# Kernel tuning notes

Hardware: AMD Instinct MI355X
Metric: run time of the kernel (lower is better)

Reference implementation:

```python
import jax, jax.numpy as jnp
import numpy as np
from jax import lax

EPS = 1e-5

def setup_inputs() -> dict:
    key = jax.random.key(0)
    k1, k2, k3 = jax.random.split(key, 3)
    B, S, D, W = 4, 4096, 2048, 4
    x = jax.random.normal(k1, (B, S, D), dtype=jnp.float32)
    norm_weight = jnp.ones((D,), dtype=jnp.float32)
    conv_weight = jax.random.normal(k2, (D, W), dtype=jnp.float32) * (1.0 / np.sqrt(W))
    proj_weight = jax.random.normal(k3, (2, D), dtype=jnp.float32) * (1.0 / np.sqrt(D))
    return {"x": x, "norm_weight": norm_weight, "conv_weight": conv_weight, "proj_weight": proj_weight}

def _rmsnorm(x, w):
    var = jnp.mean(x * x, axis=-1, keepdims=True)
    return x * lax.rsqrt(var + EPS) * w

def _causal_dw_conv_silu(h, conv_weight):
    # h: [B,S,D], conv_weight: [D,W]; causal depthwise conv along seq + silu
    B, S, D = h.shape
    W = conv_weight.shape[-1]
    hc = jnp.transpose(h, (0, 2, 1))                      # [B,D,S]
    hc = jnp.pad(hc, ((0, 0), (0, 0), (W - 1, 0)))        # left-pad for causality
    y = lax.conv_general_dilated(
        hc, conv_weight[:, None, :], window_strides=(1,), padding='VALID',
        dimension_numbers=('NCH', 'OIH', 'NCH'), feature_group_count=D)
    return jnp.transpose(jax.nn.silu(y), (0, 2, 1))       # [B,S,D]

def reference(x, norm_weight, conv_weight, proj_weight):
    B, S, D = x.shape
    h = _rmsnorm(x, norm_weight)
    h = _causal_dw_conv_silu(h, conv_weight)
    logits = jnp.einsum('bsd,od->bso', h, proj_weight)    # [B,S,2]
    gate = jax.nn.softmax(logits, axis=-1)[..., 1]        # [B,S]
    mask = gate > 0.5                                     # [B,S]
    # cumsum-index scatter-compress: selected tokens packed to the front,
    # unselected tokens routed to slot 0 which is dropped (padded to S, vs
    # data-dependent max_q in torch).
    idx = jnp.where(mask, jnp.cumsum(mask.astype(jnp.int32), axis=1), 0)  # [B,S]
    buf = jnp.zeros((B, S + 1, D), dtype=x.dtype)
    bidx = jnp.arange(B)[:, None]
    buf = buf.at[bidx, idx].set(x)
    return buf[:, 1:]
```

## Files before the change

kernel.cpp:

```cpp
#include <hip/hip_runtime.h>
#include <cstddef>

#define BATCH 4
#define SEQ   4096
#define DIM   2048
#define EPSF  1e-5f
#define TCHUNK 8
#define CPB   (SEQ / TCHUNK)
#define NBLK  (BATCH * CPB)

__device__ __forceinline__ float wave_sum(float v) {
#pragma unroll
    for (int off = 32; off > 0; off >>= 1)
        v += __shfl_down(v, off, 64);
    return v;
}

__global__ __launch_bounds__(256, 3) void mask_kernel(
    const float* __restrict__ x, const float* __restrict__ nw,
    const float* __restrict__ cw, const float* __restrict__ pw,
    unsigned short* __restrict__ tok)
{
    __shared__ float lds_ss[3][4][4];
    __shared__ float lds_acc[2][4][4];

    const int t = threadIdx.x, lane = t & 63, wid = t >> 6;
    const int G = gridDim.x;
    const int chunk = (blockIdx.x & 7) * (G >> 3) + (blockIdx.x >> 3);
    const int b  = chunk / CPB;
    const int s0 = (chunk % CPB) * TCHUNK;
    const int d0 = 4 * t, d1 = d0 + 1024;

    float cwn[8][4], pd[8];
    {
        float4 n0 = *(const float4*)(nw + d0);
        float4 n1 = *(const float4*)(nw + d1);
        float nv[8] = {n0.x, n0.y, n0.z, n0.w, n1.x, n1.y, n1.z, n1.w};
#pragma unroll
        for (int i = 0; i < 8; ++i) {
            const int d = (i < 4) ? (d0 + i) : (d1 + i - 4);
            float4 c4 = *(const float4*)(cw + 4 * d);
            cwn[i][0] = c4.x * nv[i]; cwn[i][1] = c4.y * nv[i];
            cwn[i][2] = c4.z * nv[i]; cwn[i][3] = c4.w * nv[i];
        }
        float4 a0 = *(const float4*)(pw + d0);
        float4 a1 = *(const float4*)(pw + d1);
        float4 b0 = *(const float4*)(pw + DIM + d0);
        float4 b1 = *(const float4*)(pw + DIM + d1);
        pd[0] = b0.x - a0.x; pd[1] = b0.y - a0.y; pd[2] = b0.z - a0.z; pd[3] = b0.w - a0.w;
        pd[4] = b1.x - a1.x; pd[5] = b1.y - a1.y; pd[6] = b1.z - a1.z; pd[7] = b1.w - a1.w;
    }

    const float* xb = x + (size_t)b * SEQ * DIM;
    float h1[8], h2[8], h3[8];

    {
        float wv[3][8];
#pragma unroll
        for (int w = 0; w < 3; ++w) {
            const int s = s0 - 3 + w;
            if (s >= 0) {
                float4 a = *(const float4*)(xb + (size_t)s * DIM + d0);
                float4 c = *(const float4*)(xb + (size_t)s * DIM + d1);
                wv[w][0]=a.x; wv[w][1]=a.y; wv[w][2]=a.z; wv[w][3]=a.w;
                wv[w][4]=c.x; wv[w][5]=c.y; wv[w][6]=c.z; wv[w][7]=c.w;
            } else {
#pragma unroll
                for (int i = 0; i < 8; ++i) wv[w][i] = 0.f;
            }
            float ss = 0.f;
#pragma unroll
            for (int i = 0; i < 8; ++i) ss += wv[w][i] * wv[w][i];
            ss = wave_sum(ss);
            if (lane == 0) lds_ss[2][w][wid] = ss;
        }
        __syncthreads();
#pragma unroll
        for (int w = 0; w < 3; ++w) {
            const float sum4 = lds_ss[2][w][0] + lds_ss[2][w][1]
                             + lds_ss[2][w][2] + lds_ss[2][w][3];
            const float rstd = 1.0f / sqrtf(sum4 * (1.0f / DIM) + EPSF);
            float* h = (w == 0) ? h3 : (w == 1) ? h2 : h1;
#pragma unroll
            for (int i = 0; i < 8; ++i) h[i] = wv[w][i] * rstd;
        }
    }

    int pending = -1;
#pragma unroll
    for (int g = 0; g < 2; ++g) {
        float xv[4][8];
#pragma unroll
        for (int j = 0; j < 4; ++j) {
            const int s = s0 + 4 * g + j;
            float4 a = *(const float4*)(xb + (size_t)s * DIM + d0);
            float4 c = *(const float4*)(xb + (size_t)s * DIM + d1);
            xv[j][0]=a.x; xv[j][1]=a.y; xv[j][2]=a.z; xv[j][3]=a.w;
            xv[j][4]=c.x; xv[j][5]=c.y; xv[j][6]=c.z; xv[j][7]=c.w;
        }
#pragma unroll
        for (int j = 0; j < 4; ++j) {
            float ss = 0.f;
#pragma unroll
            for (int i = 0; i < 8; ++i) ss += xv[j][i] * xv[j][i];
            ss = wave_sum(ss);
            if (lane == 0) lds_ss[g][j][wid] = ss;
        }
        __syncthreads();
        if (pending >= 0 && t < 4) {
            const float a = lds_acc[pending][t][0] + lds_acc[pending][t][1]
                          + lds_acc[pending][t][2] + lds_acc[pending][t][3];
            tok[b * SEQ + s0 + 4 * pending + t] = (a > 0.f) ? 0x8000 : 0;
        }
#pragma unroll
        for (int j = 0; j < 4; ++j) {
            const float sum4 = lds_ss[g][j][0] + lds_ss[g][j][1]
                             + lds_ss[g][j][2] + lds_ss[g][j][3];
            const float rstd = 1.0f / sqrtf(sum4 * (1.0f / DIM) + EPSF);
            float acc = 0.f;
#pragma unroll
            for (int i = 0; i < 8; ++i) {
                const float hc = xv[j][i] * rstd;
                const float y = cwn[i][0] * h3[i] + cwn[i][1] * h2[i]
                              + cwn[i][2] * h1[i] + cwn[i][3] * hc;
                const float sig = 1.0f / (1.0f + __expf(-y));
                acc += (y * sig) * pd[i];
                h3[i] = h2[i]; h2[i] = h1[i]; h1[i] = hc;
            }
            acc = wave_sum(acc);
            if (lane == 0) lds_acc[g][j][wid] = acc;
        }
        pending = g;
    }
    __syncthreads();
    if (t < 4) {
        const float a = lds_acc[1][t][0] + lds_acc[1][t][1]
                      + lds_acc[1][t][2] + lds_acc[1][t][3];
        tok[b * SEQ + s0 + 4 + t] = (a > 0.f) ? 0x8000 : 0;
    }
}

__global__ __launch_bounds__(256) void scan_kernel(unsigned short* __restrict__ tok)
{
    const int b = blockIdx.x, t = threadIdx.x;
    const int PER = SEQ / 256;
    __shared__ int wtot[4];

    int m[PER], tot = 0;
#pragma unroll
    for (int i = 0; i < PER; ++i) {
        m[i] = tok[b * SEQ + t * PER + i] >> 15;
        tot += m[i];
    }
    const int lane = t & 63, wid = t >> 6;
    int inc = tot;
#pragma unroll
    for (int off = 1; off < 64; off <<= 1) {
        int v = __shfl_up(inc, off, 64);
        if (lane >= off) inc += v;
    }
    if (lane == 63) wtot[wid] = inc;
    __syncthreads();
    int pref = inc - tot;
    for (int w = 0; w < wid; ++w) pref += wtot[w];

    int run = pref;
#pragma unroll
    for (int i = 0; i < PER; ++i) {
        run += m[i];
        tok[b * SEQ + t * PER + i] = (unsigned short)((m[i] << 15) | run);
    }
}

__global__ __launch_bounds__(256) void scatter_kernel(
    const float* __restrict__ x, const unsigned short* __restrict__ tok,
    float* __restrict__ out)
{
    const int b = blockIdx.x / SEQ;
    const int s = blockIdx.x - b * SEQ;
    const int t = threadIdx.x;
    const unsigned v    = tok[b * SEQ + s];
    const int     nsel  = tok[b * SEQ + SEQ - 1] & 0x7FFF;
    const int     p     = v & 0x7FFF;
    const int     dest  = (v & 0x8000u) ? (p - 1) : (nsel + s - p);
    float* o = out + ((size_t)b * SEQ + dest) * DIM;
    if (v & 0x8000u) {
        const float* src = x + ((size_t)b * SEQ + s) * DIM;
        *(float4*)(o + 4 * t)        = *(const float4*)(src + 4 * t);
        *(float4*)(o + 4 * t + 1024) = *(const float4*)(src + 4 * t + 1024);
    } else {
        const float4 z = make_float4(0.f, 0.f, 0.f, 0.f);
        *(float4*)(o + 4 * t)        = z;
        *(float4*)(o + 4 * t + 1024) = z;
    }
}

extern "C" void kernel_launch(void* const* d_in, const int* in_sizes, int n_in,
                              void* d_out, int out_size, void* d_ws, size_t ws_size,
                              hipStream_t stream) {
    const float* x  = (const float*)d_in[0];
    const float* nw = (const float*)d_in[1];
    const float* cw = (const float*)d_in[2];
    const float* pw = (const float*)d_in[3];
    float* out = (float*)d_out;

    unsigned short* tok = (unsigned short*)d_ws;

    mask_kernel<<<NBLK, 256, 0, stream>>>(x, nw, cw, pw, tok);
    scan_kernel<<<BATCH, 256, 0, stream>>>(tok);
    scatter_kernel<<<BATCH * SEQ, 256, 0, stream>>>(x, tok, out);
}
```

Before: 265.0 us.

## Fuse mask, scan and scatter via decoupled-lookback single-pass prefix scan

Merges the mask computation, the prefix scan and the scatter into one kernel. Chunks are handed out in order through an atomic ticket and use a decoupled-lookback chain to find each chunk's output offset. Selected rows are then written straight from registers, so x is not read a second time. A separate kernel zeroes only the tail rows past the selected count. The change adds spin-waiting on predecessor chunks, a memset launch, and lower occupancy (launch bounds 2 blocks) in exchange for removing a full re-read of x and two extra kernel passes.

Result: slower. 471.2 us (+77.8%).

```diff
diff --git a/kernel.cpp b/kernel.cpp
--- a/kernel.cpp
+++ b/kernel.cpp
@@ -9,28 +9,42 @@
 #define CPB   (SEQ / TCHUNK)
 #define NBLK  (BATCH * CPB)
 
+#define AGGF 0x40000000u
+#define INCF 0x80000000u
+#define VALM 0xFFFFu
+
 __device__ __forceinline__ float wave_sum(float v) {
 #pragma unroll
     for (int off = 32; off > 0; off >>= 1)
         v += __shfl_down(v, off, 64);
     return v;
 }
-
-__global__ __launch_bounds__(256, 3) void mask_kernel(
+__device__ __forceinline__ int wave_sum_i(int v) {
+#pragma unroll
+    for (int off = 32; off > 0; off >>= 1)
+        v += __shfl_down(v, off, 64);
+    return v;
+}
+
+__global__ __launch_bounds__(256, 2) void fused_kernel(
     const float* __restrict__ x, const float* __restrict__ nw,
     const float* __restrict__ cw, const float* __restrict__ pw,
-    unsigned short* __restrict__ tok)
+    unsigned int* __restrict__ ws, float* __restrict__ out)
 {
-    __shared__ float lds_ss[3][4][4];
-    __shared__ float lds_acc[2][4][4];
+    __shared__ float lds_ss[11][4];
+    __shared__ float lds_acc[8][4];
+    __shared__ unsigned int lds_chunk;
+    __shared__ unsigned int lds_excl;
+
+    unsigned int* ticket = ws;
+    unsigned int* nsel   = ws + 1;
+    unsigned int* chain  = ws + 8;
 
     const int t = threadIdx.x, lane = t & 63, wid = t >> 6;
-    const int G = gridDim.x;
-    const int chunk = (blockIdx.x & 7) * (G >> 3) + (blockIdx.x >> 3);
-    const int b  = chunk / CPB;
-    const int s0 = (chunk % CPB) * TCHUNK;
+
+    if (t == 0) lds_chunk = atomicAdd(ticket, 1u);
+
     const int d0 = 4 * t, d1 = d0 + 1024;
-
     float cwn[8][4], pd[8];
     {
         float4 n0 = *(const float4*)(nw + d0);
@@ -50,148 +64,173 @@
         pd[0] = b0.x - a0.x; pd[1] = b0.y - a0.y; pd[2] = b0.z - a0.z; pd[3] = b0.w - a0.w;
         pd[4] = b1.x - a1.x; pd[5] = b1.y - a1.y; pd[6] = b1.z - a1.z; pd[7] = b1.w - a1.w;
     }
-
+    __syncthreads();
+    const unsigned chunk = lds_chunk;
+    const int b    = (int)(chunk >> 9);
+    const int cidx = (int)(chunk & (CPB - 1));
+    const int s0   = cidx * TCHUNK;
     const float* xb = x + (size_t)b * SEQ * DIM;
-    float h1[8], h2[8], h3[8];
-
-    {
-        float wv[3][8];
-#pragma unroll
-        for (int w = 0; w < 3; ++w) {
-            const int s = s0 - 3 + w;
-            if (s >= 0) {
-                float4 a = *(const float4*)(xb + (size_t)s * DIM + d0);
-                float4 c = *(const float4*)(xb + (size_t)s * DIM + d1);
-                wv[w][0]=a.x; wv[w][1]=a.y; wv[w][2]=a.z; wv[w][3]=a.w;
-                wv[w][4]=c.x; wv[w][5]=c.y; wv[w][6]=c.z; wv[w][7]=c.w;
-            } else {
-#pragma unroll
-                for (int i = 0; i < 8; ++i) wv[w][i] = 0.f;
-            }
-            float ss = 0.f;
-#pragma unroll
-            for (int i = 0; i < 8; ++i) ss += wv[w][i] * wv[w][i];
-            ss = wave_sum(ss);
-            if (lane == 0) lds_ss[2][w][wid] = ss;
-        }
-        __syncthreads();
-#pragma unroll
-        for (int w = 0; w < 3; ++w) {
-            const float sum4 = lds_ss[2][w][0] + lds_ss[2][w][1]
-                             + lds_ss[2][w][2] + lds_ss[2][w][3];
-            const float rstd = 1.0f / sqrtf(sum4 * (1.0f / DIM) + EPSF);
-            float* h = (w == 0) ? h3 : (w == 1) ? h2 : h1;
-#pragma unroll
-            for (int i = 0; i < 8; ++i) h[i] = wv[w][i] * rstd;
-        }
-    }
-
-    int pending = -1;
-#pragma unroll
-    for (int g = 0; g < 2; ++g) {
-        float xv[4][8];
-#pragma unroll
-        for (int j = 0; j < 4; ++j) {
-            const int s = s0 + 4 * g + j;
+
+    float wv[3][8];
+#pragma unroll
+    for (int w = 0; w < 3; ++w) {
+        const int s = s0 - 3 + w;
+        if (s >= 0) {
             float4 a = *(const float4*)(xb + (size_t)s * DIM + d0);
             float4 c = *(const float4*)(xb + (size_t)s * DIM + d1);
-            xv[j][0]=a.x; xv[j][1]=a.y; xv[j][2]=a.z; xv[j][3]=a.w;
-            xv[j][4]=c.x; xv[j][5]=c.y; xv[j][6]=c.z; xv[j][7]=c.w;
-        }
-#pragma unroll
-        for (int j = 0; j < 4; ++j) {
-            float ss = 0.f;
-#pragma unroll
-            for (int i = 0; i < 8; ++i) ss += xv[j][i] * xv[j][i];
-            ss = wave_sum(ss);
-            if (lane == 0) lds_ss[g][j][wid] = ss;
-        }
-        __syncthreads();
-        if (pending >= 0 && t < 4) {
-            const float a = lds_acc[pending][t][0] + lds_acc[pending][t][1]
-                          + lds_acc[pending][t][2] + lds_acc[pending][t][3];
-            tok[b * SEQ + s0 + 4 * pending + t] = (a > 0.f) ? 0x8000 : 0;
-        }
-#pragma unroll
-        for (int j = 0; j < 4; ++j) {
-            const float sum4 = lds_ss[g][j][0] + lds_ss[g][j][1]
-                             + lds_ss[g][j][2] + lds_ss[g][j][3];
-            const float rstd = 1.0f / sqrtf(sum4 * (1.0f / DIM) + EPSF);
-            float acc = 0.f;
-#pragma unroll
-            for (int i = 0; i < 8; ++i) {
-                const float hc = xv[j][i] * rstd;
-                const float y = cwn[i][0] * h3[i] + cwn[i][1] * h2[i]
-                              + cwn[i][2] * h1[i] + cwn[i][3] * hc;
-                const float sig = 1.0f / (1.0f + __expf(-y));
-                acc += (y * sig) * pd[i];
-                h3[i] = h2[i]; h2[i] = h1[i]; h1[i] = hc;
+            wv[w][0]=a.x; wv[w][1]=a.y; wv[w][2]=a.z; wv[w][3]=a.w;
+            wv[w][4]=c.x; wv[w][5]=c.y; wv[w][6]=c.z; wv[w][7]=c.w;
+        } else {
+#pragma unroll
+            for (int i = 0; i < 8; ++i) wv[w][i] = 0.f;
+        }
+    }
+    float xv[8][8];
+#pragma unroll
+    for (int j = 0; j < 8; ++j) {
+        const int s = s0 + j;
+        float4 a = *(const float4*)(xb + (size_t)s * DIM + d0);
+        float4 c = *(const float4*)(xb + (size_t)s * DIM + d1);
+        xv[j][0]=a.x; xv[j][1]=a.y; xv[j][2]=a.z; xv[j][3]=a.w;
+        xv[j][4]=c.x; xv[j][5]=c.y; xv[j][6]=c.z; xv[j][7]=c.w;
+    }
+
+#pragma unroll
+    for (int w = 0; w < 3; ++w) {
+        float ss = 0.f;
+#pragma unroll
+        for (int i = 0; i < 8; ++i) ss += wv[w][i] * wv[w][i];
+        ss = wave_sum(ss);
+        if (lane == 0) lds_ss[w][wid] = ss;
+    }
+#pragma unroll
+    for (int j = 0; j < 8; ++j) {
+        float ss = 0.f;
+#pragma unroll
+        for (int i = 0; i < 8; ++i) ss += xv[j][i] * xv[j][i];
+        ss = wave_sum(ss);
+        if (lane == 0) lds_ss[3 + j][wid] = ss;
+    }
+    __syncthreads();
+
+    float h1[8], h2[8], h3[8];
+#pragma unroll
+    for (int w = 0; w < 3; ++w) {
+        const float sum4 = lds_ss[w][0] + lds_ss[w][1]
+                         + lds_ss[w][2] + lds_ss[w][3];
+        const float rstd = 1.0f / sqrtf(sum4 * (1.0f / DIM) + EPSF);
+        float* h = (w == 0) ? h3 : (w == 1) ? h2 : h1;
+#pragma unroll
+        for (int i = 0; i < 8; ++i) h[i] = wv[w][i] * rstd;
+    }
+
+#pragma unroll
+    for (int j = 0; j < 8; ++j) {
+        const float sum4 = lds_ss[3 + j][0] + lds_ss[3 + j][1]
+                         + lds_ss[3 + j][2] + lds_ss[3 + j][3];
+        const float rstd = 1.0f / sqrtf(sum4 * (1.0f / DIM) + EPSF);
+        float acc = 0.f;
+#pragma unroll
+        for (int i = 0; i < 8; ++i) {
+            const float hc = xv[j][i] * rstd;
+            const float y = cwn[i][0] * h3[i] + cwn[i][1] * h2[i]
+                          + cwn[i][2] * h1[i] + cwn[i][3] * hc;
+            const float sig = 1.0f / (1.0f + __expf(-y));
+            acc += (y * sig) * pd[i];
+            h3[i] = h2[i]; h2[i] = h1[i]; h1[i] = hc;
+        }
+        acc = wave_sum(acc);
+        if (lane == 0) lds_acc[j][wid] = acc;
+    }
+    __syncthreads();
+
+    unsigned mbits = 0; int cnt = 0;
+#pragma unroll
+    for (int j = 0; j < 8; ++j) {
+        const float a = lds_acc[j][0] + lds_acc[j][1]
+                      + lds_acc[j][2] + lds_acc[j][3];
+        if (a > 0.f) { mbits |= (1u << j); ++cnt; }
+    }
+
+    if (cidx == 0) {
+        if (t == 0) {
+            lds_excl = 0;
+            __hip_atomic_store(&chain[chunk], (unsigned)cnt | INCF,
+                               __ATOMIC_RELEASE, __HIP_MEMORY_SCOPE_AGENT);
+        }
+    } else {
+        if (t == 0)
+            __hip_atomic_store(&chain[chunk], (unsigned)cnt | AGGF,
+                               __ATOMIC_RELEASE, __HIP_MEMORY_SCOPE_AGENT);
+        if (wid == 0) {
+            int excl = 0;
+            int back = cidx;
+            const unsigned int* chb = chain + ((size_t)b << 9);
+            while (back > 0) {
+                const int look = back - 1 - lane;
+                unsigned v = 0;
+                if (look >= 0) {
+                    do {
+                        v = __hip_atomic_load(chb + look, __ATOMIC_ACQUIRE,
+                                              __HIP_MEMORY_SCOPE_AGENT);
+                    } while (!(v & (AGGF | INCF)));
+                }
+                const unsigned long long bal = __ballot((v & INCF) != 0);
+                const int val = (int)(v & VALM);
+                if (bal) {
+                    const int k = (int)__ffsll((unsigned long long)bal) - 1;
+                    excl += wave_sum_i((lane <= k) ? val : 0);
+                    back = 0;
+                } else {
+                    excl += wave_sum_i((look >= 0) ? val : 0);
+                    back -= 64;
+                }
             }
-            acc = wave_sum(acc);
-            if (lane == 0) lds_acc[g][j][wid] = acc;
-        }
-        pending = g;
-    }
-    __syncthreads();
-    if (t < 4) {
-        const float a = lds_acc[1][t][0] + lds_acc[1][t][1]
-                      + lds_acc[1][t][2] + lds_acc[1][t][3];
-        tok[b * SEQ + s0 + 4 + t] = (a > 0.f) ? 0x8000 : 0;
-    }
-}
-
-__global__ __launch_bounds__(256) void scan_kernel(unsigned short* __restrict__ tok)
+            if (lane == 0) {
+                lds_excl = (unsigned)excl;
+                __hip_atomic_store(&chain[chunk], (unsigned)(excl + cnt) | INCF,
+                                   __ATOMIC_RELEASE, __HIP_MEMORY_SCOPE_AGENT);
+                if (cidx == CPB - 1) nsel[b] = (unsigned)(excl + cnt);
+            }
+        }
+    }
+    __syncthreads();
+
+    if (mbits) {
+        int dest = (int)lds_excl;
+#pragma unroll
+        for (int j = 0; j < 8; ++j) {
+            if (mbits & (1u << j)) {
+                float* o = out + ((size_t)b * SEQ + dest) * DIM;
+                float4 a = {xv[j][0], xv[j][1], xv[j][2], xv[j][3]};
+                float4 c = {xv[j][4], xv[j][5], xv[j][6], xv[j][7]};
+                *(float4*)(o + d0) = a;
+                *(float4*)(o + d1) = c;
+                ++dest;
+            }
+        }
+    }
+}
+
+__global__ __launch_bounds__(256) void zeros_kernel(
+    const unsigned int* __restrict__ ws, float* __restrict__ out)
 {
-    const int b = blockIdx.x, t = threadIdx.x;
-    const int PER = SEQ / 256;
-    __shared__ int wtot[4];
-
-    int m[PER], tot = 0;
-#pragma unroll
-    for (int i = 0; i < PER; ++i) {
-        m[i] = tok[b * SEQ + t * PER + i] >> 15;
-        tot += m[i];
-    }
-    const int lane = t & 63, wid = t >> 6;
-    int inc = tot;
-#pragma unroll
-    for (int off = 1; off < 64; off <<= 1) {
-        int v = __shfl_up(inc, off, 64);
-        if (lane >= off) inc += v;
-    }
-    if (lane == 63) wtot[wid] = inc;
-    __syncthreads();
-    int pref = inc - tot;
-    for (int w = 0; w < wid; ++w) pref += wtot[w];
-
-    int run = pref;
-#pragma unroll
-    for (int i = 0; i < PER; ++i) {
-        run += m[i];
-        tok[b * SEQ + t * PER + i] = (unsigned short)((m[i] << 15) | run);
-    }
-}
-
-__global__ __launch_bounds__(256) void scatter_kernel(
-    const float* __restrict__ x, const unsigned short* __restrict__ tok,
-    float* __restrict__ out)
-{
-    const int b = blockIdx.x / SEQ;
-    const int s = blockIdx.x - b * SEQ;
+    const int bpb = SEQ / 8;
+    const int b   = blockIdx.x / bpb;
+    const int r0  = (blockIdx.x % bpb) * 8;
+    const int n   = (int)ws[1 + b];
+    if (r0 + 8 <= n) return;
     const int t = threadIdx.x;
-    const unsigned v    = tok[b * SEQ + s];
-    const int     nsel  = tok[b * SEQ + SEQ - 1] & 0x7FFF;
-    const int     p     = v & 0x7FFF;
-    const int     dest  = (v & 0x8000u) ? (p - 1) : (nsel + s - p);
-    float* o = out + ((size_t)b * SEQ + dest) * DIM;
-    if (v & 0x8000u) {
-        const float* src = x + ((size_t)b * SEQ + s) * DIM;
-        *(float4*)(o + 4 * t)        = *(const float4*)(src + 4 * t);
-        *(float4*)(o + 4 * t + 1024) = *(const float4*)(src + 4 * t + 1024);
-    } else {
-        const float4 z = make_float4(0.f, 0.f, 0.f, 0.f);
-        *(float4*)(o + 4 * t)        = z;
-        *(float4*)(o + 4 * t + 1024) = z;
+    const float4 z = make_float4(0.f, 0.f, 0.f, 0.f);
+    float* ob = out + (size_t)b * SEQ * DIM;
+#pragma unroll
+    for (int j = 0; j < 8; ++j) {
+        const int r = r0 + j;
+        if (r >= n) {
+            float* o = ob + (size_t)r * DIM;
+            *(float4*)(o + 4 * t)        = z;
+            *(float4*)(o + 4 * t + 1024) = z;
+        }
     }
 }
 
@@ -204,9 +243,9 @@
     const float* pw = (const float*)d_in[3];
     float* out = (float*)d_out;
 
-    unsigned short* tok = (unsigned short*)d_ws;
-
-    mask_kernel<<<NBLK, 256, 0, stream>>>(x, nw, cw, pw, tok);
-    scan_kernel<<<BATCH, 256, 0, stream>>>(tok);
-    scatter_kernel<<<BATCH * SEQ, 256, 0, stream>>>(x, tok, out);
-}
+    unsigned int* ws = (unsigned int*)d_ws;
+
+    hipMemsetAsync(d_ws, 0, (8 + NBLK) * sizeof(unsigned int), stream);
+    fused_kernel<<<NBLK, 256, 0, stream>>>(x, nw, cw, pw, ws, out);
+    zeros_kernel<<<BATCH * (SEQ / 8), 256, 0, stream>>>(ws, out);
+}
```

## Replace scan kernel with per-chunk counts and in-scatter prefix reduction

Applied to the files above, without the earlier changes.

The mask kernel now writes one word per 8-token chunk holding the selection count and bitmask, computed with a ballot. The separate single-block-per-batch scan kernel is removed. The scatter kernel now runs one block per chunk and recomputes the chunk's prefix by reducing the 512 chunk counts of its batch. Each scatter block handles 8 rows instead of 1, which cuts one launch and the serial scan, at the cost of redundant prefix reductions in every block.

After: 263.4 us. About the same (-0.6%).

```diff
diff --git a/kernel.cpp b/kernel.cpp
--- a/kernel.cpp
+++ b/kernel.cpp
@@ -15,11 +15,17 @@
         v += __shfl_down(v, off, 64);
     return v;
 }
+__device__ __forceinline__ int wave_sum_i(int v) {
+#pragma unroll
+    for (int off = 32; off > 0; off >>= 1)
+        v += __shfl_down(v, off, 64);
+    return v;
+}
 
 __global__ __launch_bounds__(256, 3) void mask_kernel(
     const float* __restrict__ x, const float* __restrict__ nw,
     const float* __restrict__ cw, const float* __restrict__ pw,
-    unsigned short* __restrict__ tok)
+    unsigned int* __restrict__ cnt)
 {
     __shared__ float lds_ss[3][4][4];
     __shared__ float lds_acc[2][4][4];
@@ -86,7 +92,6 @@
         }
     }
 
-    int pending = -1;
 #pragma unroll
     for (int g = 0; g < 2; ++g) {
         float xv[4][8];
@@ -107,11 +112,6 @@
             if (lane == 0) lds_ss[g][j][wid] = ss;
         }
         __syncthreads();
-        if (pending >= 0 && t < 4) {
-            const float a = lds_acc[pending][t][0] + lds_acc[pending][t][1]
-                          + lds_acc[pending][t][2] + lds_acc[pending][t][3];
-            tok[b * SEQ + s0 + 4 * pending + t] = (a > 0.f) ? 0x8000 : 0;
-        }
 #pragma unroll
         for (int j = 0; j < 4; ++j) {
             const float sum4 = lds_ss[g][j][0] + lds_ss[g][j][1]
@@ -130,68 +130,74 @@
             acc = wave_sum(acc);
             if (lane == 0) lds_acc[g][j][wid] = acc;
         }
-        pending = g;
     }
     __syncthreads();
-    if (t < 4) {
-        const float a = lds_acc[1][t][0] + lds_acc[1][t][1]
-                      + lds_acc[1][t][2] + lds_acc[1][t][3];
-        tok[b * SEQ + s0 + 4 + t] = (a > 0.f) ? 0x8000 : 0;
-    }
-}
-
-__global__ __launch_bounds__(256) void scan_kernel(unsigned short* __restrict__ tok)
-{
-    const int b = blockIdx.x, t = threadIdx.x;
-    const int PER = SEQ / 256;
-    __shared__ int wtot[4];
-
-    int m[PER], tot = 0;
-#pragma unroll
-    for (int i = 0; i < PER; ++i) {
-        m[i] = tok[b * SEQ + t * PER + i] >> 15;
-        tot += m[i];
-    }
-    const int lane = t & 63, wid = t >> 6;
-    int inc = tot;
-#pragma unroll
-    for (int off = 1; off < 64; off <<= 1) {
-        int v = __shfl_up(inc, off, 64);
-        if (lane >= off) inc += v;
-    }
-    if (lane == 63) wtot[wid] = inc;
-    __syncthreads();
-    int pref = inc - tot;
-    for (int w = 0; w < wid; ++w) pref += wtot[w];
-
-    int run = pref;
-#pragma unroll
-    for (int i = 0; i < PER; ++i) {
-        run += m[i];
-        tok[b * SEQ + t * PER + i] = (unsigned short)((m[i] << 15) | run);
+
+    if (wid == 0) {
+        int sel = 0;
+        if (lane < 8) {
+            const int g = lane >> 2, j = lane & 3;
+            const float a = lds_acc[g][j][0] + lds_acc[g][j][1]
+                          + lds_acc[g][j][2] + lds_acc[g][j][3];
+            sel = (a > 0.f) ? 1 : 0;
+        }
+        const unsigned long long bal = __ballot(sel);
+        if (lane == 0)
+            cnt[chunk] = (unsigned)__popcll(bal) | ((unsigned)(bal & 0xFFull) << 16);
     }
 }
 
 __global__ __launch_bounds__(256) void scatter_kernel(
-    const float* __restrict__ x, const unsigned short* __restrict__ tok,
+    const float* __restrict__ x, const unsigned int* __restrict__ cnt,
     float* __restrict__ out)
 {
-    const int b = blockIdx.x / SEQ;
-    const int s = blockIdx.x - b * SEQ;
-    const int t = threadIdx.x;
-    const unsigned v    = tok[b * SEQ + s];
-    const int     nsel  = tok[b * SEQ + SEQ - 1] & 0x7FFF;
-    const int     p     = v & 0x7FFF;
-    const int     dest  = (v & 0x8000u) ? (p - 1) : (nsel + s - p);
-    float* o = out + ((size_t)b * SEQ + dest) * DIM;
-    if (v & 0x8000u) {
-        const float* src = x + ((size_t)b * SEQ + s) * DIM;
-        *(float4*)(o + 4 * t)        = *(const float4*)(src + 4 * t);
-        *(float4*)(o + 4 * t + 1024) = *(const float4*)(src + 4 * t + 1024);
-    } else {
-        const float4 z = make_float4(0.f, 0.f, 0.f, 0.f);
-        *(float4*)(o + 4 * t)        = z;
-        *(float4*)(o + 4 * t + 1024) = z;
+    __shared__ unsigned int lds_r[4];
+    const int blk  = blockIdx.x;
+    const int b    = blk >> 9;
+    const int cidx = blk & (CPB - 1);
+    const int t = threadIdx.x, lane = t & 63, wid = t >> 6;
+
+    const unsigned int* cb = cnt + b * CPB;
+    const unsigned vown = cb[cidx];
+    const unsigned bits = vown >> 16;
+
+    const unsigned u0 = cb[t];
+    const unsigned u1 = cb[256 + t];
+
+    const int s0 = cidx * TCHUNK;
+    const float* xb = x + (size_t)b * SEQ * DIM;
+    const int d0 = 4 * t, d1 = d0 + 1024;
+    const float4 z = make_float4(0.f, 0.f, 0.f, 0.f);
+    float4 ra[TCHUNK], rc[TCHUNK];
+#pragma unroll
+    for (int j = 0; j < TCHUNK; ++j) {
+        if ((bits >> j) & 1) {
+            const float* src = xb + (size_t)(s0 + j) * DIM;
+            ra[j] = *(const float4*)(src + d0);
+            rc[j] = *(const float4*)(src + d1);
+        } else { ra[j] = z; rc[j] = z; }
+    }
+
+    const int c0 = (int)(u0 & 0xFFFFu), c1 = (int)(u1 & 0xFFFFu);
+    int pack = (((t < cidx) ? c0 : 0) + ((256 + t < cidx) ? c1 : 0))
+             + ((c0 + c1) << 16);
+    pack = wave_sum_i(pack);
+    if (lane == 0) lds_r[wid] = (unsigned)pack;
+    __syncthreads();
+    const unsigned tot = lds_r[0] + lds_r[1] + lds_r[2] + lds_r[3];
+    const int pre  = (int)(tot & 0xFFFFu);
+    const int nsel = (int)(tot >> 16);
+
+    float* ob = out + (size_t)b * SEQ * DIM;
+#pragma unroll
+    for (int j = 0; j < TCHUNK; ++j) {
+        const int incl = __popc(bits & ((2u << j) - 1u));
+        const int p    = pre + incl;
+        const int sel  = (bits >> j) & 1;
+        const int dest = sel ? (p - 1) : (nsel + s0 + j - p);
+        float* o = ob + (size_t)dest * DIM;
+        *(float4*)(o + d0) = ra[j];
+        *(float4*)(o + d1) = rc[j];
     }
 }
 
@@ -204,9 +210,7 @@
     const float* pw = (const float*)d_in[3];
     float* out = (float*)d_out;
 
-    unsigned short* tok = (unsigned short*)d_ws;
-
-    mask_kernel<<<NBLK, 256, 0, stream>>>(x, nw, cw, pw, tok);
-    scan_kernel<<<BATCH, 256, 0, stream>>>(tok);
-    scatter_kernel<<<BATCH * SEQ, 256, 0, stream>>>(x, tok, out);
-}
+    unsigned int* cnt = (unsigned int*)d_ws;
+    mask_kernel<<<NBLK, 256, 0, stream>>>(x, nw, cw, pw, cnt);
+    scatter_kernel<<<NBLK, 256, 0, stream>>>(x, cnt, out);
+}
```
